# Optimization experiments

Hardware: AMD Instinct MI355X
Metric: run time of the kernel (lower is better)

The kernel has to match this reference:

```python
import jax, jax.numpy as jnp
import numpy as np
import math

DIM = 2048
D_STATE = 64
EXPAND = 2
CHUNK = 64
HEADDIM = 64
D_CONV = 4
D_INNER = EXPAND * DIM          # 4096
NHEADS = D_INNER // HEADDIM     # 64


def _segsum(x):
    """x: (..., T) -> (..., T, T); out[i,j] = sum_{k=j+1}^{i} x[k] for i>=j else -inf."""
    T = x.shape[-1]
    keep = jnp.tril(jnp.ones((T, T), bool), -1)          # strictly lower
    seg = jnp.cumsum(jnp.where(keep, x[..., None], 0.0), axis=-2)
    valid = jnp.tril(jnp.ones((T, T), bool))
    return jnp.where(valid, seg, -jnp.inf)


def _ssd(X, A, B, C, block):
    """Chunkwise SSD scan (Mamba-2 Listing 1). X:(b,L,h,p) A:(b,L,h) B,C:(b,L,h,n)."""
    b, L, h, p = X.shape
    n = B.shape[-1]
    c = L // block
    X = X.reshape(b, c, block, h, p)
    A = A.reshape(b, c, block, h)
    B = B.reshape(b, c, block, h, n)
    C = C.reshape(b, c, block, h, n)
    A = jnp.transpose(A, (0, 3, 1, 2))                    # (b,h,c,l)
    A_cum = jnp.cumsum(A, axis=-1)
    # intra-chunk (diagonal block) output
    L_intra = jnp.exp(_segsum(A))                         # (b,h,c,l,s)
    Y_diag = jnp.einsum('bclhn,bcshn,bhcls,bcshp->bclhp', C, B, L_intra, X)
    # per-chunk final states
    decay_states = jnp.exp(A_cum[..., -1:] - A_cum)       # (b,h,c,l)
    states = jnp.einsum('bclhn,bhcl,bclhp->bchpn', B, decay_states, X)
    states = jnp.concatenate([jnp.zeros_like(states[:, :1]), states], axis=1)
    # inter-chunk recurrence across chunk boundaries
    chunk_end = jnp.pad(A_cum[..., -1], ((0, 0), (0, 0), (1, 0)))  # (b,h,c+1)
    decay_chunk = jnp.exp(_segsum(chunk_end))             # (b,h,c+1,c+1)
    new_states = jnp.einsum('bhzc,bchpn->bzhpn', decay_chunk, states)
    states_per_chunk = new_states[:, :-1]
    # off-diagonal contribution from carried-in states
    state_decay_out = jnp.exp(A_cum)                      # (b,h,c,l)
    Y_off = jnp.einsum('bclhn,bchpn,bhcl->bclhp', C, states_per_chunk, state_decay_out)
    return (Y_diag + Y_off).reshape(b, L, h, p)


def setup_inputs() -> dict:
    key = jax.random.key(0)
    ks = jax.random.split(key, 6)
    b, l = 2, 2048
    x = jax.random.normal(ks[0], (b, l, DIM), jnp.float32)
    proj_out = 2 * D_INNER + 2 * D_STATE + NHEADS
    in_proj_w = jax.random.normal(ks[1], (proj_out, DIM), jnp.float32) / math.sqrt(DIM)
    conv_w = jax.random.normal(ks[2], (D_INNER, 1, D_CONV), jnp.float32) / math.sqrt(D_CONV)
    conv_b = jnp.zeros((D_INNER,), jnp.float32)
    out_proj_w = jax.random.normal(ks[3], (DIM, D_INNER), jnp.float32) / math.sqrt(D_INNER)
    A_log = jnp.zeros((NHEADS,), jnp.float32)
    D_skip = jnp.ones((D_INNER,), jnp.float32)
    u = jax.random.uniform(ks[4], (NHEADS,), jnp.float32)
    dt = jnp.clip(jnp.exp(u * (math.log(0.1) - math.log(0.001)) + math.log(0.001)), 1e-4, None)
    dt_bias = dt + jnp.log(-jnp.expm1(-dt))
    return dict(x=x, in_proj_w=in_proj_w, conv_w=conv_w, conv_b=conv_b,
                out_proj_w=out_proj_w, A_log=A_log, D_skip=D_skip, dt_bias=dt_bias)


def reference(x, in_proj_w, conv_w, conv_b, out_proj_w, A_log, D_skip, dt_bias):
    b, l, _ = x.shape
    proj = x @ in_proj_w.T
    splits = [D_INNER, 2 * D_INNER, 2 * D_INNER + D_STATE, 2 * D_INNER + 2 * D_STATE]
    x_branch, z, B_in, C_in, dt = jnp.split(proj, splits, axis=-1)
    # causal depthwise conv1d (torch pads both sides then slices [:l] == left-pad only)
    xc = jnp.transpose(x_branch, (0, 2, 1))               # (b, d_inner, l)
    xc = jax.lax.conv_general_dilated(
        xc, conv_w, (1,), [(D_CONV - 1, 0)],
        dimension_numbers=('NCH', 'OIH', 'NCH'), feature_group_count=D_INNER)
    xc = xc + conv_b[None, :, None]
    x_act = jax.nn.silu(jnp.transpose(xc, (0, 2, 1)))     # (b,l,d_inner)
    x_h = x_act.reshape(b, l, NHEADS, HEADDIM)
    dt_f = jax.nn.softplus(dt + dt_bias)                  # (b,l,h)
    A_f = -jnp.exp(A_log)                                 # (h,)
    X_disc = x_h * dt_f[..., None]
    A_disc = A_f[None, None, :] * dt_f
    B_b = jnp.broadcast_to(B_in[:, :, None, :], (b, l, NHEADS, D_STATE))
    C_b = jnp.broadcast_to(C_in[:, :, None, :], (b, l, NHEADS, D_STATE))
    Y = _ssd(X_disc, A_disc, B_b, C_b, CHUNK)             # (b,l,h,p)
    y = Y.reshape(b, l, D_INNER) + D_skip * x_act
    y = y * jax.nn.silu(z)
    return y @ out_proj_w.T
```

## Files before the change

### kernel.cpp

```cpp
#include <hip/hip_runtime.h>

typedef unsigned short u16;
typedef unsigned int   u32;
typedef __attribute__((ext_vector_type(8))) short bf16x8;
typedef __attribute__((ext_vector_type(4))) float f32x4;

__device__ __forceinline__ u16 f2bf(float f){
  u32 u = __builtin_bit_cast(u32, f);
  u32 r = (u + 0x7FFFu + ((u >> 16) & 1u)) >> 16;
  return (u16)r;
}
__device__ __forceinline__ float bf2f(u16 h){
  u32 u = ((u32)h) << 16;
  return __builtin_bit_cast(float, u);
}
__device__ __forceinline__ void llds16(const u16* g, u16* l){
  __builtin_amdgcn_global_load_lds((const __attribute__((address_space(1))) void*)g,
                                   (__attribute__((address_space(3))) void*)l, 16, 0, 0);
}

#define FENCE asm volatile("" ::: "memory")
#define BAR   do { FENCE; __builtin_amdgcn_s_barrier(); FENCE; } while (0)
#define LGKM0 do { asm volatile("s_waitcnt lgkmcnt(0)" ::: "memory"); __builtin_amdgcn_sched_barrier(0); } while (0)
#define VMC6  do { asm volatile("s_waitcnt vmcnt(6)" ::: "memory"); __builtin_amdgcn_sched_barrier(0); } while (0)
#define VMC0  do { asm volatile("s_waitcnt vmcnt(0)" ::: "memory"); __builtin_amdgcn_sched_barrier(0); } while (0)

#define MFMAQ(mh, nh)                                                         \
  _Pragma("unroll") for (int i = 0; i < 4; i++)                               \
    _Pragma("unroll") for (int j = 0; j < 2; j++)                             \
      _Pragma("unroll") for (int kb = 0; kb < 2; kb++)                        \
        acc[mh][nh][i][j] = __builtin_amdgcn_mfma_f32_16x16x32_bf16(          \
            a[i][kb], bfr[j][kb], acc[mh][nh][i][j], 0, 0, 0);

__global__ __launch_bounds__(256) void cast4(const float* __restrict__ in, u16* __restrict__ out, int n4){
  int i = blockIdx.x * 256 + threadIdx.x;
  if (i >= n4) return;
  float4 v = ((const float4*)in)[i];
  u32 lo = (u32)f2bf(v.x) | ((u32)f2bf(v.y) << 16);
  u32 hi = (u32)f2bf(v.z) | ((u32)f2bf(v.w) << 16);
  ((uint2*)out)[i] = make_uint2(lo, hi);
}

__global__ __launch_bounds__(256) void castpad_w1(const float* __restrict__ in, u16* __restrict__ out){
  int i = blockIdx.x * 256 + threadIdx.x;
  if (i >= 8448 * 512) return;
  int nrow = i >> 9;
  float4 v = make_float4(0.f, 0.f, 0.f, 0.f);
  if (nrow < 8384) v = ((const float4*)in)[i];
  u32 lo = (u32)f2bf(v.x) | ((u32)f2bf(v.y) << 16);
  u32 hi = (u32)f2bf(v.z) | ((u32)f2bf(v.w) << 16);
  ((uint2*)out)[i] = make_uint2(lo, hi);
}

template<bool OUTF32>
__global__ __launch_bounds__(512, 2)
void gemm8p(const u16* __restrict__ A, const u16* __restrict__ Bm, void* __restrict__ Cout,
            int NYT, int N, int K)
{
  __shared__ u16 L[65536];
  const int tid = threadIdx.x;
  const int lane = tid & 63, wid = tid >> 6;
  const int wr = wid >> 2, wc = wid & 3;
  const int lr = lane & 15, lk8 = (lane >> 4) * 8;
  const int lterm = lr * 32 + (lk8 ^ ((lr & 8) << 1));
  const int nwg = gridDim.x;
  const int lid = blockIdx.x;
  const int q = nwg >> 3;
  const int swz = (lid & 7) * q + (lid >> 3);
  const int ty = swz % NYT, tx = swz / NYT;
  const size_t bm0 = (size_t)ty * 256;
  const size_t bn0 = (size_t)tx * 256;
  const int NT = K >> 6;

  const int si0 = wid * 2, si1 = si0 + 1;
  const int rsub = lane >> 2;
  const int cg = (lane & 3) ^ ((lane & 32) ? 2 : 0);
  const int rh0 = (si0 >> 1) * 16 + rsub, kc0 = (si0 & 1) * 32 + cg * 8;
  const int rh1 = (si1 >> 1) * 16 + rsub, kc1 = (si1 & 1) * 32 + cg * 8;

  auto stage = [&](int isA, int h, int tt) {
    const int slot = (tt & 1) * 4 + (isA ? 0 : 2) + h;
    const u16* gb = (isA ? A : Bm) + ((isA ? bm0 : bn0) + (size_t)h * 128) * (size_t)K;
    u16* lb = L + slot * 8192 + lane * 8;
    llds16(gb + (size_t)rh0 * K + (size_t)tt * 64 + kc0, lb + si0 * 512);
    llds16(gb + (size_t)rh1 * K + (size_t)tt * 64 + kc1, lb + si1 * 512);
  };

  bf16x8 a[4][2], bfr[2][2];
  f32x4 acc[2][2][4][2] = {};

  auto rdA = [&](int p, int mh) {
    #pragma unroll
    for (int i = 0; i < 4; i++)
      #pragma unroll
      for (int kb = 0; kb < 2; kb++)
        a[i][kb] = *(const bf16x8*)&L[(p * 4 + mh) * 8192 + ((wr * 4 + i) * 2 + kb) * 512 + lterm];
  };
  auto rdB = [&](int p, int nh) {
    #pragma unroll
    for (int j = 0; j < 2; j++)
      #pragma unroll
      for (int kb = 0; kb < 2; kb++)
        bfr[j][kb] = *(const bf16x8*)&L[(p * 4 + 2 + nh) * 8192 + ((wc * 2 + j) * 2 + kb) * 512 + lterm];
  };

  stage(1, 0, 0); stage(1, 1, 0); stage(0, 0, 0); stage(0, 1, 0);
  stage(1, 0, 1); stage(1, 1, 1); stage(0, 0, 1);
  VMC6;
  BAR;

  for (int t = 0; t < NT; ++t) {
    const int p = t & 1;
    const bool s1 = (t + 1 < NT);
    const bool s2 = (t + 2 < NT);
    rdA(p, 0); rdB(p, 0);
    if (s1) stage(0, 1, t + 1);
    BAR; LGKM0;
    __builtin_amdgcn_s_setprio(1); MFMAQ(0, 0); __builtin_amdgcn_s_setprio(0);
    BAR;
    rdB(p, 1);
    if (s2) stage(1, 0, t + 2);
    BAR; LGKM0;
    __builtin_amdgcn_s_setprio(1); MFMAQ(0, 1); __builtin_amdgcn_s_setprio(0);
    BAR;
    rdA(p, 1); rdB(p, 0);
    BAR; LGKM0;
    __builtin_amdgcn_s_setprio(1); MFMAQ(1, 0); __builtin_amdgcn_s_setprio(0);
    BAR;
    rdB(p, 1);
    if (s2) { stage(1, 1, t + 2); stage(0, 0, t + 2); }
    if (t < NT - 2) { VMC6; } else { VMC0; }
    BAR; LGKM0;
    __builtin_amdgcn_s_setprio(1); MFMAQ(1, 1); __builtin_amdgcn_s_setprio(0);
    BAR;
  }

  const int lg4 = (lane >> 4) * 4;
  #pragma unroll
  for (int mh = 0; mh < 2; mh++)
    #pragma unroll
    for (int nh = 0; nh < 2; nh++)
      #pragma unroll
      for (int i = 0; i < 4; i++)
        #pragma unroll
        for (int j = 0; j < 2; j++) {
          size_t col = bn0 + nh * 128 + wc * 32 + j * 16 + lr;
          #pragma unroll
          for (int r2 = 0; r2 < 4; r2++) {
            size_t row = bm0 + mh * 128 + wr * 64 + i * 16 + lg4 + r2;
            float v = acc[mh][nh][i][j][r2];
            if (OUTF32) ((float*)Cout)[row * N + col] = v;
            else        ((u16*)Cout)[row * N + col] = f2bf(v);
          }
        }
}

__global__ __launch_bounds__(512, 2)
void gemm2sk(const u16* __restrict__ A, const u16* __restrict__ Bm, float* __restrict__ P,
             int NYT, int N, int KLEN, int LDK)
{
  __shared__ u16 L[65536];
  const int tid = threadIdx.x;
  const int lane = tid & 63, wid = tid >> 6;
  const int wr = wid >> 2, wc = wid & 3;
  const int lr = lane & 15, lk8 = (lane >> 4) * 8;
  const int lterm = lr * 32 + (lk8 ^ ((lr & 8) << 1));
  const int lid = blockIdx.x;
  const int ks = lid >> 7;
  const int lid2 = lid & 127;
  const int q = 128 >> 3;
  const int swz = (lid2 & 7) * q + (lid2 >> 3);
  const int ty = swz % NYT, tx = swz / NYT;
  const size_t bm0 = (size_t)ty * 256;
  const size_t bn0 = (size_t)tx * 256;
  const int NT = KLEN >> 6;
  const size_t koff = (size_t)ks * KLEN;
  float* Pout = P + (size_t)ks * 8388608;

  const int si0 = wid * 2, si1 = si0 + 1;
  const int rsub = lane >> 2;
  const int cg = (lane & 3) ^ ((lane & 32) ? 2 : 0);
  const int rh0 = (si0 >> 1) * 16 + rsub, kc0 = (si0 & 1) * 32 + cg * 8;
  const int rh1 = (si1 >> 1) * 16 + rsub, kc1 = (si1 & 1) * 32 + cg * 8;

  auto stage = [&](int isA, int h, int tt) {
    const int slot = (tt & 1) * 4 + (isA ? 0 : 2) + h;
    const u16* gb = (isA ? A : Bm) + ((isA ? bm0 : bn0) + (size_t)h * 128) * (size_t)LDK + koff;
    u16* lb = L + slot * 8192 + lane * 8;
    llds16(gb + (size_t)rh0 * LDK + (size_t)tt * 64 + kc0, lb + si0 * 512);
    llds16(gb + (size_t)rh1 * LDK + (size_t)tt * 64 + kc1, lb + si1 * 512);
  };

  bf16x8 a[4][2], bfr[2][2];
  f32x4 acc[2][2][4][2] = {};

  auto rdA = [&](int p, int mh) {
    #pragma unroll
    for (int i = 0; i < 4; i++)
      #pragma unroll
      for (int kb = 0; kb < 2; kb++)
        a[i][kb] = *(const bf16x8*)&L[(p * 4 + mh) * 8192 + ((wr * 4 + i) * 2 + kb) * 512 + lterm];
  };
  auto rdB = [&](int p, int nh) {
    #pragma unroll
    for (int j = 0; j < 2; j++)
      #pragma unroll
      for (int kb = 0; kb < 2; kb++)
        bfr[j][kb] = *(const bf16x8*)&L[(p * 4 + 2 + nh) * 8192 + ((wc * 2 + j) * 2 + kb) * 512 + lterm];
  };

  stage(1, 0, 0); stage(1, 1, 0); stage(0, 0, 0); stage(0, 1, 0);
  stage(1, 0, 1); stage(1, 1, 1); stage(0, 0, 1);
  VMC6;
  BAR;

  for (int t = 0; t < NT; ++t) {
    const int p = t & 1;
    const bool s1 = (t + 1 < NT);
    const bool s2 = (t + 2 < NT);
    rdA(p, 0); rdB(p, 0);
    if (s1) stage(0, 1, t + 1);
    BAR; LGKM0;
    __builtin_amdgcn_s_setprio(1); MFMAQ(0, 0); __builtin_amdgcn_s_setprio(0);
    BAR;
    rdB(p, 1);
    if (s2) stage(1, 0, t + 2);
    BAR; LGKM0;
    __builtin_amdgcn_s_setprio(1); MFMAQ(0, 1); __builtin_amdgcn_s_setprio(0);
    BAR;
    rdA(p, 1); rdB(p, 0);
    BAR; LGKM0;
    __builtin_amdgcn_s_setprio(1); MFMAQ(1, 0); __builtin_amdgcn_s_setprio(0);
    BAR;
    rdB(p, 1);
    if (s2) { stage(1, 1, t + 2); stage(0, 0, t + 2); }
    if (t < NT - 2) { VMC6; } else { VMC0; }
    BAR; LGKM0;
    __builtin_amdgcn_s_setprio(1); MFMAQ(1, 1); __builtin_amdgcn_s_setprio(0);
    BAR;
  }

  const int lg4 = (lane >> 4) * 4;
  #pragma unroll
  for (int mh = 0; mh < 2; mh++)
    #pragma unroll
    for (int nh = 0; nh < 2; nh++)
      #pragma unroll
      for (int i = 0; i < 4; i++)
        #pragma unroll
        for (int j = 0; j < 2; j++) {
          size_t col = bn0 + nh * 128 + wc * 32 + j * 16 + lr;
          #pragma unroll
          for (int r2 = 0; r2 < 4; r2++) {
            size_t row = bm0 + mh * 128 + wr * 64 + i * 16 + lg4 + r2;
            Pout[row * N + col] = acc[mh][nh][i][j][r2];
          }
        }
}

__global__ __launch_bounds__(256)
void addp(const float* __restrict__ p0, const float* __restrict__ p1, float* __restrict__ out){
  int i = blockIdx.x * 256 + threadIdx.x;
  float4 a = ((const float4*)p0)[i];
  float4 b = ((const float4*)p1)[i];
  ((float4*)out)[i] = make_float4(a.x + b.x, a.y + b.y, a.z + b.z, a.w + b.w);
}

__global__ __launch_bounds__(256)
void postproj(const u16* __restrict__ proj, const float* __restrict__ dt_bias,
              float* __restrict__ dtf, u16* __restrict__ Bb, u16* __restrict__ Cb)
{
  int i = blockIdx.x * 256 + threadIdx.x;
  if (i >= 4096 * 64) return;
  int bl = i >> 6, hh = i & 63;
  const u16* pr = proj + (size_t)bl * 8448;
  float dv = bf2f(pr[8320 + hh]) + dt_bias[hh];
  dtf[i] = dv > 20.f ? dv : log1pf(__expf(dv));
  Bb[i] = pr[8192 + hh];
  Cb[i] = pr[8256 + hh];
}

__global__ __launch_bounds__(256)
void conv_silu(const u16* __restrict__ proj, const float* __restrict__ cw,
               const float* __restrict__ cb, const float* __restrict__ dtf,
               u16* __restrict__ xact, u16* __restrict__ Xd)
{
  int bl = blockIdx.x;
  int d0 = blockIdx.y * 2048 + threadIdx.x * 8;
  int l = bl & 2047;
  float a[8];
  {
    float4 b0 = *(const float4*)&cb[d0];
    float4 b1 = *(const float4*)&cb[d0 + 4];
    a[0]=b0.x; a[1]=b0.y; a[2]=b0.z; a[3]=b0.w; a[4]=b1.x; a[5]=b1.y; a[6]=b1.z; a[7]=b1.w;
  }
  float4 wv[8];
  #pragma unroll
  for (int e = 0; e < 8; e++) wv[e] = *(const float4*)&cw[(size_t)(d0 + e) * 4];
  #pragma unroll
  for (int t = 0; t < 4; t++) {
    if (l + t >= 3) {
      const u16* row = proj + (size_t)(bl - 3 + t) * 8448 + d0;
      uint4 rv = *(const uint4*)row;
      const u16* re = (const u16*)&rv;
      #pragma unroll
      for (int e = 0; e < 8; e++) {
        float w = (t==0) ? wv[e].x : (t==1) ? wv[e].y : (t==2) ? wv[e].z : wv[e].w;
        a[e] += w * bf2f(re[e]);
      }
    }
  }
  float dt = dtf[(size_t)bl * 64 + (d0 >> 6)];
  u16 xo[8], xdo[8];
  #pragma unroll
  for (int e = 0; e < 8; e++) {
    float v = a[e];
    float sil = v / (1.f + __expf(-v));
    xo[e]  = f2bf(sil);
    xdo[e] = f2bf(sil * dt);
  }
  *(uint4*)(xact + (size_t)bl * 4096 + d0) = *(const uint4*)xo;
  *(uint4*)(Xd   + (size_t)bl * 4096 + d0) = *(const uint4*)xdo;
}

__global__ __launch_bounds__(256)
void ssd_states(const u16* __restrict__ Xd, const u16* __restrict__ Bg,
                const float* __restrict__ dtf, const float* __restrict__ A_log,
                u16* __restrict__ Stg, float* __restrict__ dtot)
{
  const int wg = blockIdx.x;
  const int b = wg >> 11, h = wg & 63;
  const int c = (wg >> 6) & 31;
  const int bl0 = b * 2048 + c * 64;
  __shared__ u16 Bt[64*64], Xts[64*64];
  __shared__ float avals[64], Acum[64], Adec[64];
  const int tid = threadIdx.x, wave = tid >> 6, lane = tid & 63;
  const int qi = (wave >> 1) * 32, qj = (wave & 1) * 32;
  const int lr = lane & 15, lk8 = (lane >> 4) * 8, lg = (lane >> 4) * 4;
  const float negA = -__expf(A_log[h]);

  if (tid < 64) avals[tid] = negA * dtf[(size_t)(bl0 + tid) * 64 + h];
  __syncthreads();
  if (tid < 64) { float s = 0.f; for (int j = 0; j <= tid; j++) s += avals[j]; Acum[tid] = s; }
  __syncthreads();
  if (tid < 64) Adec[tid] = __expf(Acum[63] - Acum[tid]);
  if (tid == 0) dtot[wg] = __expf(Acum[63]);
  __syncthreads();
  {
    int s = tid & 63, c0 = (tid >> 6) * 16;
    float dec = Adec[s];
    const u16* bs = Bg + (size_t)(bl0 + s) * 64 + c0;
    const u16* xs = Xd + (size_t)(bl0 + s) * 4096 + h * 64 + c0;
    #pragma unroll
    for (int j = 0; j < 16; j++) {
      Bt[(c0 + j) * 64 + s] = bs[j];
      Xts[(c0 + j) * 64 + s] = f2bf(bf2f(xs[j]) * dec);
    }
  }
  __syncthreads();
  f32x4 accst[2][2] = {};
  #pragma unroll
  for (int kk = 0; kk < 64; kk += 32) {
    bf16x8 xsf[2], btf[2];
    #pragma unroll
    for (int t = 0; t < 2; t++) {
      xsf[t] = *(const bf16x8*)&Xts[(qi + t * 16 + lr) * 64 + kk + lk8];
      btf[t] = *(const bf16x8*)&Bt [(qj + t * 16 + lr) * 64 + kk + lk8];
    }
    #pragma unroll
    for (int ti = 0; ti < 2; ti++)
      #pragma unroll
      for (int tj = 0; tj < 2; tj++)
        accst[ti][tj] = __builtin_amdgcn_mfma_f32_16x16x32_bf16(xsf[ti], btf[tj], accst[ti][tj], 0, 0, 0);
  }
  u16* So = Stg + (size_t)wg * 4096;
  #pragma unroll
  for (int ti = 0; ti < 2; ti++)
    #pragma unroll
    for (int tj = 0; tj < 2; tj++) {
      int nn = qj + tj * 16 + lr;
      #pragma unroll
      for (int r2 = 0; r2 < 4; r2++) {
        int pp = qi + ti * 16 + lg + r2;
        So[pp * 64 + nn] = f2bf(accst[ti][tj][r2]);
      }
    }
}

__global__ __launch_bounds__(256)
void ssd_scan(u16* __restrict__ Stg, const float* __restrict__ dtot)
{
  const int gid = blockIdx.x * 256 + threadIdx.x;
  const int bh = gid >> 12;
  const int pn = gid & 4095;
  const int b = bh >> 6, h = bh & 63;
  float R = 0.f;
  for (int c = 0; c < 32; ++c) {
    const int whc = b * 2048 + c * 64 + h;
    size_t idx = (size_t)whc * 4096 + pn;
    float st = bf2f(Stg[idx]);
    Stg[idx] = f2bf(R);
    R = R * dtot[whc] + st;
  }
}

__global__ __launch_bounds__(256)
void ssd_y(const u16* __restrict__ Xd, const u16* __restrict__ Bg, const u16* __restrict__ Cg,
           const float* __restrict__ dtf, const float* __restrict__ A_log,
           const u16* __restrict__ xact, const u16* __restrict__ proj,
           const float* __restrict__ Dskip, const u16* __restrict__ Stg,
           u16* __restrict__ Yout)
{
  const int wg = blockIdx.x;
  const int b = wg >> 11, h = wg & 63;
  const int c = (wg >> 6) & 31;
  const int bl0 = b * 2048 + c * 64;
  __shared__ u16 Cb[64*64], Bb[64*64], Xt[64*64], Sb[64*64], P[64*64];
  __shared__ float avals[64], Acum[64], Aexp[64];
  const int tid = threadIdx.x, wave = tid >> 6, lane = tid & 63;
  const int qi = (wave >> 1) * 32, qj = (wave & 1) * 32;
  const int lr = lane & 15, lk8 = (lane >> 4) * 8, lg = (lane >> 4) * 4;
  const float negA = -__expf(A_log[h]);

  if (tid < 64) avals[tid] = negA * dtf[(size_t)(bl0 + tid) * 64 + h];
  __syncthreads();
  if (tid < 64) { float s = 0.f; for (int j = 0; j <= tid; j++) s += avals[j]; Acum[tid] = s; }
  __syncthreads();
  if (tid < 64) Aexp[tid] = __expf(Acum[tid]);
  __syncthreads();
  {
    int l = tid >> 2, n0 = (tid & 3) * 16;
    const uint4* s0 = (const uint4*)(Cg + (size_t)(bl0 + l) * 64 + n0);
    *(uint4*)&Cb[l * 64 + n0] = s0[0]; *(uint4*)&Cb[l * 64 + n0 + 8] = s0[1];
    const uint4* s1 = (const uint4*)(Bg + (size_t)(bl0 + l) * 64 + n0);
    *(uint4*)&Bb[l * 64 + n0] = s1[0]; *(uint4*)&Bb[l * 64 + n0 + 8] = s1[1];
    int s = tid & 63, c0 = (tid >> 6) * 16;
    const u16* xs = Xd + (size_t)(bl0 + s) * 4096 + h * 64 + c0;
    #pragma unroll
    for (int j = 0; j < 16; j++) Xt[(c0 + j) * 64 + s] = xs[j];
    const uint4* sp = (const uint4*)(Stg + (size_t)wg * 4096 + tid * 16);
    *(uint4*)&Sb[tid * 16] = sp[0]; *(uint4*)&Sb[tid * 16 + 8] = sp[1];
  }
  __syncthreads();
  f32x4 accs[2][2] = {}; f32x4 accy[2][2] = {};
  #pragma unroll
  for (int kk = 0; kk < 64; kk += 32) {
    bf16x8 cf[2], bfr[2], sf[2];
    #pragma unroll
    for (int t = 0; t < 2; t++) {
      cf[t]  = *(const bf16x8*)&Cb[(qi + t * 16 + lr) * 64 + kk + lk8];
      bfr[t] = *(const bf16x8*)&Bb[(qj + t * 16 + lr) * 64 + kk + lk8];
      sf[t]  = *(const bf16x8*)&Sb[(qj + t * 16 + lr) * 64 + kk + lk8];
    }
    #pragma unroll
    for (int ti = 0; ti < 2; ti++)
      #pragma unroll
      for (int tj = 0; tj < 2; tj++) {
        accs[ti][tj] = __builtin_amdgcn_mfma_f32_16x16x32_bf16(cf[ti], bfr[tj], accs[ti][tj], 0, 0, 0);
        accy[ti][tj] = __builtin_amdgcn_mfma_f32_16x16x32_bf16(cf[ti], sf[tj],  accy[ti][tj], 0, 0, 0);
      }
  }
  #pragma unroll
  for (int ti = 0; ti < 2; ti++)
    #pragma unroll
    for (int tj = 0; tj < 2; tj++) {
      int j = qj + tj * 16 + lr;
      float Aj = Acum[j];
      #pragma unroll
      for (int r2 = 0; r2 < 4; r2++) {
        int i = qi + ti * 16 + lg + r2;
        float v = (i >= j) ? accs[ti][tj][r2] * __expf(Acum[i] - Aj) : 0.f;
        P[i * 64 + j] = f2bf(v);
        accy[ti][tj][r2] *= Aexp[i];
      }
    }
  __syncthreads();
  #pragma unroll
  for (int kk = 0; kk < 64; kk += 32) {
    bf16x8 pf[2], xf_[2];
    #pragma unroll
    for (int t = 0; t < 2; t++) {
      pf[t]  = *(const bf16x8*)&P [(qi + t * 16 + lr) * 64 + kk + lk8];
      xf_[t] = *(const bf16x8*)&Xt[(qj + t * 16 + lr) * 64 + kk + lk8];
    }
    #pragma unroll
    for (int ti = 0; ti < 2; ti++)
      #pragma unroll
      for (int tj = 0; tj < 2; tj++)
        accy[ti][tj] = __builtin_amdgcn_mfma_f32_16x16x32_bf16(pf[ti], xf_[tj], accy[ti][tj], 0, 0, 0);
  }
  #pragma unroll
  for (int ti = 0; ti < 2; ti++)
    #pragma unroll
    for (int tj = 0; tj < 2; tj++) {
      int pcol = qj + tj * 16 + lr;
      int d = h * 64 + pcol;
      float dsk = Dskip[d];
      #pragma unroll
      for (int r2 = 0; r2 < 4; r2++) {
        int lrow = qi + ti * 16 + lg + r2;
        size_t bl = (size_t)bl0 + lrow;
        float y = accy[ti][tj][r2];
        float xa = bf2f(xact[bl * 4096 + d]);
        float z = bf2f(proj[bl * 8448 + 4096 + d]);
        float sz = z / (1.f + __expf(-z));
        Yout[bl * 4096 + d] = f2bf((y + dsk * xa) * sz);
      }
    }
}

__global__ __launch_bounds__(256)
void ssd_kernel(const u16* __restrict__ Xd, const u16* __restrict__ Bg, const u16* __restrict__ Cg,
                const float* __restrict__ dtf, const float* __restrict__ A_log,
                const u16* __restrict__ xact, const u16* __restrict__ proj,
                const float* __restrict__ Dskip, u16* __restrict__ Yout)
{
  const int bh = blockIdx.x;
  const int b = bh >> 6, h = bh & 63;
  __shared__ float S[64 * 64];
  __shared__ u16 Cb[64*64], Bb[64*64], Bt[64*64], Xt[64*64], Xts[64*64], Sb[64*64], P[64*64];
  __shared__ float avals[64], Acum[64], Adec[64], Aexp[64];
  const int tid = threadIdx.x, wave = tid >> 6, lane = tid & 63;
  const int qi = (wave >> 1) * 32, qj = (wave & 1) * 32;
  const int lr = lane & 15, lk8 = (lane >> 4) * 8, lg = (lane >> 4) * 4;
  const float negA = -__expf(A_log[h]);

  for (int i = tid; i < 4096; i += 256) S[i] = 0.f;

  for (int c = 0; c < 32; ++c) {
    const int bl0 = b * 2048 + c * 64;
    __syncthreads();
    if (tid < 64) avals[tid] = negA * dtf[(size_t)(bl0 + tid) * 64 + h];
    __syncthreads();
    if (tid < 64) { float s = 0.f; for (int j = 0; j <= tid; j++) s += avals[j]; Acum[tid] = s; }
    __syncthreads();
    if (tid < 64) { float At = Acum[63]; Adec[tid] = __expf(At - Acum[tid]); Aexp[tid] = __expf(Acum[tid]); }
    __syncthreads();
    {
      int l = tid >> 2, n0 = (tid & 3) * 16;
      const uint4* s0 = (const uint4*)(Cg + (size_t)(bl0 + l) * 64 + n0);
      *(uint4*)&Cb[l * 64 + n0] = s0[0]; *(uint4*)&Cb[l * 64 + n0 + 8] = s0[1];
      const uint4* s1 = (const uint4*)(Bg + (size_t)(bl0 + l) * 64 + n0);
      *(uint4*)&Bb[l * 64 + n0] = s1[0]; *(uint4*)&Bb[l * 64 + n0 + 8] = s1[1];
      int s = tid & 63, c0 = (tid >> 6) * 16;
      float dec = Adec[s];
      const u16* bs = Bg + (size_t)(bl0 + s) * 64 + c0;
      const u16* xs = Xd + (size_t)(bl0 + s) * 4096 + h * 64 + c0;
      #pragma unroll
      for (int j = 0; j < 16; j++) {
        Bt[(c0 + j) * 64 + s] = bs[j];
        u16 xv = xs[j];
        Xt[(c0 + j) * 64 + s] = xv;
        Xts[(c0 + j) * 64 + s] = f2bf(bf2f(xv) * dec);
      }
      int p = tid >> 2, m0 = (tid & 3) * 16;
      #pragma unroll
      for (int j = 0; j < 16; j++) Sb[p * 64 + m0 + j] = f2bf(S[p * 64 + m0 + j]);
    }
    __syncthreads();
    f32x4 accs[2][2] = {}; f32x4 accy[2][2] = {};
    #pragma unroll
    for (int kk = 0; kk < 64; kk += 32) {
      bf16x8 cf[2], bfr[2], sf[2];
      #pragma unroll
      for (int t = 0; t < 2; t++) {
        cf[t]  = *(const bf16x8*)&Cb[(qi + t * 16 + lr) * 64 + kk + lk8];
        bfr[t] = *(const bf16x8*)&Bb[(qj + t * 16 + lr) * 64 + kk + lk8];
        sf[t]  = *(const bf16x8*)&Sb[(qj + t * 16 + lr) * 64 + kk + lk8];
      }
      #pragma unroll
      for (int ti = 0; ti < 2; ti++)
        #pragma unroll
        for (int tj = 0; tj < 2; tj++) {
          accs[ti][tj] = __builtin_amdgcn_mfma_f32_16x16x32_bf16(cf[ti], bfr[tj], accs[ti][tj], 0, 0, 0);
          accy[ti][tj] = __builtin_amdgcn_mfma_f32_16x16x32_bf16(cf[ti], sf[tj],  accy[ti][tj], 0, 0, 0);
        }
    }
    #pragma unroll
    for (int ti = 0; ti < 2; ti++)
      #pragma unroll
      for (int tj = 0; tj < 2; tj++) {
        int j = qj + tj * 16 + lr;
        float Aj = Acum[j];
        #pragma unroll
        for (int r2 = 0; r2 < 4; r2++) {
          int i = qi + ti * 16 + lg + r2;
          float v = (i >= j) ? accs[ti][tj][r2] * __expf(Acum[i] - Aj) : 0.f;
          P[i * 64 + j] = f2bf(v);
          accy[ti][tj][r2] *= Aexp[i];
        }
      }
    __syncthreads();
    f32x4 accst[2][2] = {};
    #pragma unroll
    for (int kk = 0; kk < 64; kk += 32) {
      bf16x8 pf[2], xf_[2], xsf[2], btf[2];
      #pragma unroll
      for (int t = 0; t < 2; t++) {
        pf[t]  = *(const bf16x8*)&P  [(qi + t * 16 + lr) * 64 + kk + lk8];
        xf_[t] = *(const bf16x8*)&Xt [(qj + t * 16 + lr) * 64 + kk + lk8];
        xsf[t] = *(const bf16x8*)&Xts[(qi + t * 16 + lr) * 64 + kk + lk8];
        btf[t] = *(const bf16x8*)&Bt [(qj + t * 16 + lr) * 64 + kk + lk8];
      }
      #pragma unroll
      for (int ti = 0; ti < 2; ti++)
        #pragma unroll
        for (int tj = 0; tj < 2; tj++) {
          accy[ti][tj]  = __builtin_amdgcn_mfma_f32_16x16x32_bf16(pf[ti],  xf_[tj], accy[ti][tj],  0, 0, 0);
          accst[ti][tj] = __builtin_amdgcn_mfma_f32_16x16x32_bf16(xsf[ti], btf[tj], accst[ti][tj], 0, 0, 0);
        }
    }
    float dtot = Aexp[63];
    #pragma unroll
    for (int ti = 0; ti < 2; ti++)
      #pragma unroll
      for (int tj = 0; tj < 2; tj++) {
        int nn = qj + tj * 16 + lr;
        #pragma unroll
        for (int r2 = 0; r2 < 4; r2++) {
          int pp = qi + ti * 16 + lg + r2;
          int idx = pp * 64 + nn;
          S[idx] = dtot * S[idx] + accst[ti][tj][r2];
        }
      }
    #pragma unroll
    for (int ti = 0; ti < 2; ti++)
      #pragma unroll
      for (int tj = 0; tj < 2; tj++) {
        int pcol = qj + tj * 16 + lr;
        int d = h * 64 + pcol;
        float dsk = Dskip[d];
        #pragma unroll
        for (int r2 = 0; r2 < 4; r2++) {
          int lrow = qi + ti * 16 + lg + r2;
          size_t bl = (size_t)bl0 + lrow;
          float y = accy[ti][tj][r2];
          float xa = bf2f(xact[bl * 4096 + d]);
          float z = bf2f(proj[bl * 8448 + 4096 + d]);
          float sz = z / (1.f + __expf(-z));
          Yout[bl * 4096 + d] = f2bf((y + dsk * xa) * sz);
        }
      }
  }
}

extern "C" void kernel_launch(void* const* d_in, const int* in_sizes, int n_in,
                              void* d_out, int out_size, void* d_ws, size_t ws_size,
                              hipStream_t stream) {
  const float* x    = (const float*)d_in[0];
  const float* w1   = (const float*)d_in[1];
  const float* cw   = (const float*)d_in[2];
  const float* cbv  = (const float*)d_in[3];
  const float* w2   = (const float*)d_in[4];
  const float* alog = (const float*)d_in[5];
  const float* dsk  = (const float*)d_in[6];
  const float* dtb  = (const float*)d_in[7];
  float* out = (float*)d_out;

  char* ws = (char*)d_ws;
  u16*  x_bf  = (u16*)(ws + 0);
  u16*  w1p   = (u16*)(ws + 16777216);
  u16*  w2b   = (u16*)(ws + 51380224);
  u16*  proj  = (u16*)(ws + 68157440);
  float* dtf  = (float*)(ws + 137363456);
  u16*  Bbf   = (u16*)(ws + 138412032);
  u16*  Cbf   = (u16*)(ws + 138936320);
  u16*  xact  = (u16*)(ws + 139460608);
  u16*  Xdd   = (u16*)(ws + 173015040);
  u16*  yin   = (u16*)(ws + 206569472);
  u16*  Stg   = (u16*)(ws + 240123904);
  float* dtot = (float*)(ws + 273678336);
  const size_t NEED_PAR = 273694720ull;
  float* p0 = (float*)(ws + 68157440);
  float* p1 = p0 + 8388608;

  cast4<<<8192, 256, 0, stream>>>(x,  x_bf, 2097152);
  castpad_w1<<<16896, 256, 0, stream>>>(w1, w1p);
  cast4<<<8192, 256, 0, stream>>>(w2, w2b, 2097152);

  gemm8p<false><<<528, 512, 0, stream>>>(x_bf, w1p, proj, 16, 8448, 2048);

  postproj<<<1024, 256, 0, stream>>>(proj, dtb, dtf, Bbf, Cbf);
  conv_silu<<<dim3(4096, 2), 256, 0, stream>>>(proj, cw, cbv, dtf, xact, Xdd);

  if (ws_size >= NEED_PAR) {
    ssd_states<<<4096, 256, 0, stream>>>(Xdd, Bbf, dtf, alog, Stg, dtot);
    ssd_scan<<<2048, 256, 0, stream>>>(Stg, dtot);
    ssd_y<<<4096, 256, 0, stream>>>(Xdd, Bbf, Cbf, dtf, alog, xact, proj, dsk, Stg, yin);
  } else {
    ssd_kernel<<<128, 256, 0, stream>>>(Xdd, Bbf, Cbf, dtf, alog, xact, proj, dsk, yin);
  }

  gemm2sk<<<256, 512, 0, stream>>>(yin, w2b, p0, 16, 2048, 2048, 4096);
  addp<<<8192, 256, 0, stream>>>(p0, p1, out);
}
```

Before: 457.8 us.

## Replace input-projection GEMM with K=32 tile variant at higher occupancy

The input projection GEMM now uses a new kernel that stages 32-wide K slices instead of 64, halving LDS use to 64KB and raising launch bounds to 4 blocks per CU. The pipeline is restructured into two MFMA phases per K step with a single outstanding-load count of 3. This aims to increase occupancy and latency hiding for the 528-block launch. In exchange it doubles the number of barriers per unit of K work and may run into register pressure with four resident blocks, since the 256x256 accumulator tile is kept.

```diff
diff --git a/kernel.cpp b/kernel.cpp
--- a/kernel.cpp
+++ b/kernel.cpp
@@ -23,6 +23,7 @@
 #define BAR   do { FENCE; __builtin_amdgcn_s_barrier(); FENCE; } while (0)
 #define LGKM0 do { asm volatile("s_waitcnt lgkmcnt(0)" ::: "memory"); __builtin_amdgcn_sched_barrier(0); } while (0)
 #define VMC6  do { asm volatile("s_waitcnt vmcnt(6)" ::: "memory"); __builtin_amdgcn_sched_barrier(0); } while (0)
+#define VMC3  do { asm volatile("s_waitcnt vmcnt(3)" ::: "memory"); __builtin_amdgcn_sched_barrier(0); } while (0)
 #define VMC0  do { asm volatile("s_waitcnt vmcnt(0)" ::: "memory"); __builtin_amdgcn_sched_barrier(0); } while (0)
 
 #define MFMAQ(mh, nh)                                                         \
@@ -52,12 +53,11 @@
   ((uint2*)out)[i] = make_uint2(lo, hi);
 }
 
-template<bool OUTF32>
-__global__ __launch_bounds__(512, 2)
-void gemm8p(const u16* __restrict__ A, const u16* __restrict__ Bm, void* __restrict__ Cout,
+__global__ __launch_bounds__(512, 4)
+void gemm32(const u16* __restrict__ A, const u16* __restrict__ Bm, u16* __restrict__ Cout,
             int NYT, int N, int K)
 {
-  __shared__ u16 L[65536];
+  __shared__ u16 L[32768];
   const int tid = threadIdx.x;
   const int lane = tid & 63, wid = tid >> 6;
   const int wr = wid >> 2, wc = wid & 3;
@@ -70,7 +70,105 @@
   const int ty = swz % NYT, tx = swz / NYT;
   const size_t bm0 = (size_t)ty * 256;
   const size_t bn0 = (size_t)tx * 256;
-  const int NT = K >> 6;
+  const int NT = K >> 5;
+
+  const int cg = (lane & 3) ^ ((lane & 32) ? 2 : 0);
+  const int srow = wid * 16 + (lane >> 2);
+
+  auto stage = [&](int isB, int h, int tt) {
+    const u16* gb = (isB ? Bm : A) + ((isB ? bn0 : bm0) + (size_t)h * 128) * (size_t)K;
+    u16* lb = L + (tt & 1) * 16384 + isB * 8192 + h * 4096 + wid * 512 + lane * 8;
+    llds16(gb + (size_t)srow * K + (size_t)tt * 32 + cg * 8, lb);
+  };
+
+  bf16x8 a[4], bfr[2][2];
+  f32x4 acc[2][2][4][2] = {};
+
+  stage(0, 0, 0); stage(0, 1, 0); stage(1, 0, 0); stage(1, 1, 0);
+  stage(0, 0, 1); stage(1, 0, 1); stage(1, 1, 1);
+  VMC3;
+  BAR;
+
+  for (int u = 0; u < NT; ++u) {
+    const int p = u & 1;
+    const int pb = p * 16384;
+    #pragma unroll
+    for (int i = 0; i < 4; i++)
+      a[i] = *(const bf16x8*)&L[pb + (wr * 4 + i) * 512 + lterm];
+    #pragma unroll
+    for (int nh = 0; nh < 2; nh++)
+      #pragma unroll
+      for (int j = 0; j < 2; j++)
+        bfr[nh][j] = *(const bf16x8*)&L[pb + 8192 + nh * 4096 + (wc * 2 + j) * 512 + lterm];
+    if (u + 1 < NT) stage(0, 1, u + 1);
+    BAR; LGKM0;
+    __builtin_amdgcn_s_setprio(1);
+    #pragma unroll
+    for (int i = 0; i < 4; i++)
+      #pragma unroll
+      for (int nh = 0; nh < 2; nh++)
+        #pragma unroll
+        for (int j = 0; j < 2; j++)
+          acc[0][nh][i][j] = __builtin_amdgcn_mfma_f32_16x16x32_bf16(a[i], bfr[nh][j], acc[0][nh][i][j], 0, 0, 0);
+    __builtin_amdgcn_s_setprio(0);
+    BAR;
+    #pragma unroll
+    for (int i = 0; i < 4; i++)
+      a[i] = *(const bf16x8*)&L[pb + 4096 + (wr * 4 + i) * 512 + lterm];
+    if (u + 2 < NT) { stage(0, 0, u + 2); stage(1, 0, u + 2); stage(1, 1, u + 2); }
+    if (u < NT - 2) { VMC3; } else { VMC0; }
+    BAR; LGKM0;
+    __builtin_amdgcn_s_setprio(1);
+    #pragma unroll
+    for (int i = 0; i < 4; i++)
+      #pragma unroll
+      for (int nh = 0; nh < 2; nh++)
+        #pragma unroll
+        for (int j = 0; j < 2; j++)
+          acc[1][nh][i][j] = __builtin_amdgcn_mfma_f32_16x16x32_bf16(a[i], bfr[nh][j], acc[1][nh][i][j], 0, 0, 0);
+    __builtin_amdgcn_s_setprio(0);
+    BAR;
+  }
+
+  const int lg4 = (lane >> 4) * 4;
+  #pragma unroll
+  for (int mh = 0; mh < 2; mh++)
+    #pragma unroll
+    for (int nh = 0; nh < 2; nh++)
+      #pragma unroll
+      for (int i = 0; i < 4; i++)
+        #pragma unroll
+        for (int j = 0; j < 2; j++) {
+          size_t col = bn0 + nh * 128 + wc * 32 + j * 16 + lr;
+          #pragma unroll
+          for (int r2 = 0; r2 < 4; r2++) {
+            size_t row = bm0 + mh * 128 + wr * 64 + i * 16 + lg4 + r2;
+            Cout[row * N + col] = f2bf(acc[mh][nh][i][j][r2]);
+          }
+        }
+}
+
+__global__ __launch_bounds__(512, 2)
+void gemm2sk(const u16* __restrict__ A, const u16* __restrict__ Bm, float* __restrict__ P,
+             int NYT, int N, int KLEN, int LDK)
+{
+  __shared__ u16 L[65536];
+  const int tid = threadIdx.x;
+  const int lane = tid & 63, wid = tid >> 6;
+  const int wr = wid >> 2, wc = wid & 3;
+  const int lr = lane & 15, lk8 = (lane >> 4) * 8;
+  const int lterm = lr * 32 + (lk8 ^ ((lr & 8) << 1));
+  const int lid = blockIdx.x;
+  const int ks = lid >> 7;
+  const int lid2 = lid & 127;
+  const int q = 128 >> 3;
+  const int swz = (lid2 & 7) * q + (lid2 >> 3);
+  const int ty = swz % NYT, tx = swz / NYT;
+  const size_t bm0 = (size_t)ty * 256;
+  const size_t bn0 = (size_t)tx * 256;
+  const int NT = KLEN >> 6;
+  const size_t koff = (size_t)ks * KLEN;
+  float* Pout = P + (size_t)ks * 8388608;
 
   const int si0 = wid * 2, si1 = si0 + 1;
   const int rsub = lane >> 2;
@@ -80,10 +178,10 @@
 
   auto stage = [&](int isA, int h, int tt) {
     const int slot = (tt & 1) * 4 + (isA ? 0 : 2) + h;
-    const u16* gb = (isA ? A : Bm) + ((isA ? bm0 : bn0) + (size_t)h * 128) * (size_t)K;
+    const u16* gb = (isA ? A : Bm) + ((isA ? bm0 : bn0) + (size_t)h * 128) * (size_t)LDK + koff;
     u16* lb = L + slot * 8192 + lane * 8;
-    llds16(gb + (size_t)rh0 * K + (size_t)tt * 64 + kc0, lb + si0 * 512);
-    llds16(gb + (size_t)rh1 * K + (size_t)tt * 64 + kc1, lb + si1 * 512);
+    llds16(gb + (size_t)rh0 * LDK + (size_t)tt * 64 + kc0, lb + si0 * 512);
+    llds16(gb + (size_t)rh1 * LDK + (size_t)tt * 64 + kc1, lb + si1 * 512);
   };
 
   bf16x8 a[4][2], bfr[2][2];
@@ -148,111 +246,6 @@
           #pragma unroll
           for (int r2 = 0; r2 < 4; r2++) {
             size_t row = bm0 + mh * 128 + wr * 64 + i * 16 + lg4 + r2;
-            float v = acc[mh][nh][i][j][r2];
-            if (OUTF32) ((float*)Cout)[row * N + col] = v;
-            else        ((u16*)Cout)[row * N + col] = f2bf(v);
-          }
-        }
-}
-
-__global__ __launch_bounds__(512, 2)
-void gemm2sk(const u16* __restrict__ A, const u16* __restrict__ Bm, float* __restrict__ P,
-             int NYT, int N, int KLEN, int LDK)
-{
-  __shared__ u16 L[65536];
-  const int tid = threadIdx.x;
-  const int lane = tid & 63, wid = tid >> 6;
-  const int wr = wid >> 2, wc = wid & 3;
-  const int lr = lane & 15, lk8 = (lane >> 4) * 8;
-  const int lterm = lr * 32 + (lk8 ^ ((lr & 8) << 1));
-  const int lid = blockIdx.x;
-  const int ks = lid >> 7;
-  const int lid2 = lid & 127;
-  const int q = 128 >> 3;
-  const int swz = (lid2 & 7) * q + (lid2 >> 3);
-  const int ty = swz % NYT, tx = swz / NYT;
-  const size_t bm0 = (size_t)ty * 256;
-  const size_t bn0 = (size_t)tx * 256;
-  const int NT = KLEN >> 6;
-  const size_t koff = (size_t)ks * KLEN;
-  float* Pout = P + (size_t)ks * 8388608;
-
-  const int si0 = wid * 2, si1 = si0 + 1;
-  const int rsub = lane >> 2;
-  const int cg = (lane & 3) ^ ((lane & 32) ? 2 : 0);
-  const int rh0 = (si0 >> 1) * 16 + rsub, kc0 = (si0 & 1) * 32 + cg * 8;
-  const int rh1 = (si1 >> 1) * 16 + rsub, kc1 = (si1 & 1) * 32 + cg * 8;
-
-  auto stage = [&](int isA, int h, int tt) {
-    const int slot = (tt & 1) * 4 + (isA ? 0 : 2) + h;
-    const u16* gb = (isA ? A : Bm) + ((isA ? bm0 : bn0) + (size_t)h * 128) * (size_t)LDK + koff;
-    u16* lb = L + slot * 8192 + lane * 8;
-    llds16(gb + (size_t)rh0 * LDK + (size_t)tt * 64 + kc0, lb + si0 * 512);
-    llds16(gb + (size_t)rh1 * LDK + (size_t)tt * 64 + kc1, lb + si1 * 512);
-  };
-
-  bf16x8 a[4][2], bfr[2][2];
-  f32x4 acc[2][2][4][2] = {};
-
-  auto rdA = [&](int p, int mh) {
-    #pragma unroll
-    for (int i = 0; i < 4; i++)
-      #pragma unroll
-      for (int kb = 0; kb < 2; kb++)
-        a[i][kb] = *(const bf16x8*)&L[(p * 4 + mh) * 8192 + ((wr * 4 + i) * 2 + kb) * 512 + lterm];
-  };
-  auto rdB = [&](int p, int nh) {
-    #pragma unroll
-    for (int j = 0; j < 2; j++)
-      #pragma unroll
-      for (int kb = 0; kb < 2; kb++)
-        bfr[j][kb] = *(const bf16x8*)&L[(p * 4 + 2 + nh) * 8192 + ((wc * 2 + j) * 2 + kb) * 512 + lterm];
-  };
-
-  stage(1, 0, 0); stage(1, 1, 0); stage(0, 0, 0); stage(0, 1, 0);
-  stage(1, 0, 1); stage(1, 1, 1); stage(0, 0, 1);
-  VMC6;
-  BAR;
-
-  for (int t = 0; t < NT; ++t) {
-    const int p = t & 1;
-    const bool s1 = (t + 1 < NT);
-    const bool s2 = (t + 2 < NT);
-    rdA(p, 0); rdB(p, 0);
-    if (s1) stage(0, 1, t + 1);
-    BAR; LGKM0;
-    __builtin_amdgcn_s_setprio(1); MFMAQ(0, 0); __builtin_amdgcn_s_setprio(0);
-    BAR;
-    rdB(p, 1);
-    if (s2) stage(1, 0, t + 2);
-    BAR; LGKM0;
-    __builtin_amdgcn_s_setprio(1); MFMAQ(0, 1); __builtin_amdgcn_s_setprio(0);
-    BAR;
-    rdA(p, 1); rdB(p, 0);
-    BAR; LGKM0;
-    __builtin_amdgcn_s_setprio(1); MFMAQ(1, 0); __builtin_amdgcn_s_setprio(0);
-    BAR;
-    rdB(p, 1);
-    if (s2) { stage(1, 1, t + 2); stage(0, 0, t + 2); }
-    if (t < NT - 2) { VMC6; } else { VMC0; }
-    BAR; LGKM0;
-    __builtin_amdgcn_s_setprio(1); MFMAQ(1, 1); __builtin_amdgcn_s_setprio(0);
-    BAR;
-  }
-
-  const int lg4 = (lane >> 4) * 4;
-  #pragma unroll
-  for (int mh = 0; mh < 2; mh++)
-    #pragma unroll
-    for (int nh = 0; nh < 2; nh++)
-      #pragma unroll
-      for (int i = 0; i < 4; i++)
-        #pragma unroll
-        for (int j = 0; j < 2; j++) {
-          size_t col = bn0 + nh * 128 + wc * 32 + j * 16 + lr;
-          #pragma unroll
-          for (int r2 = 0; r2 < 4; r2++) {
-            size_t row = bm0 + mh * 128 + wr * 64 + i * 16 + lg4 + r2;
             Pout[row * N + col] = acc[mh][nh][i][j][r2];
           }
         }
@@ -678,7 +671,7 @@
   castpad_w1<<<16896, 256, 0, stream>>>(w1, w1p);
   cast4<<<8192, 256, 0, stream>>>(w2, w2b, 2097152);
 
-  gemm8p<false><<<528, 512, 0, stream>>>(x_bf, w1p, proj, 16, 8448, 2048);
+  gemm32<<<528, 512, 0, stream>>>(x_bf, w1p, proj, 16, 8448, 2048);
 
   postproj<<<1024, 256, 0, stream>>>(proj, dtb, dtf, Bbf, Cbf);
   conv_silu<<<dim3(4096, 2), 256, 0, stream>>>(proj, cw, cbv, dtf, xact, Xdd);
```

Result: slower. 1.684 ms (+267.8%).
